# Kernel tuning notes

Measured on AMD Instinct MI355X. Metric: run time of the kernel, lower is better.

The kernel has to match this reference:

```python
import jax, jax.numpy as jnp
from jax import lax
import numpy as np

WINDOW_SIZE = 11
SIGMA = 1.5  # create_windows hardcodes 1.5, ignoring self.sigma
C1 = 0.01 ** 2
C2 = 0.03 ** 2


def _gaussian(ws, sigma):
    x = np.arange(ws, dtype=np.float32)
    g = np.exp(-((x - ws // 2) ** 2) / (2.0 * sigma ** 2))
    return (g / g.sum()).astype(np.float32)


def _blur(x, window):
    # Separable depthwise Gaussian blur with 'same' symmetric padding.
    # x: [N, 1, H, W]; window: [ws]
    ws = window.shape[0]
    p = ws // 2
    dn = ('NCHW', 'OIHW', 'NCHW')
    kh = window.reshape(1, 1, ws, 1)
    kw = window.reshape(1, 1, 1, ws)
    x = lax.conv_general_dilated(x, kh, (1, 1), [(p, p), (0, 0)], dimension_numbers=dn)
    x = lax.conv_general_dilated(x, kw, (1, 1), [(0, 0), (p, p)], dimension_numbers=dn)
    return x


def setup_inputs() -> dict:
    key = jax.random.key(0)
    k1, k2 = jax.random.split(key)
    shape = (16, 1, 1024, 1024)
    img1 = jax.random.uniform(k1, shape, dtype=jnp.float32)
    img2 = jax.random.uniform(k2, shape, dtype=jnp.float32)
    window = jnp.asarray(_gaussian(WINDOW_SIZE, SIGMA))
    return {"img1": img1, "img2": img2, "window": window}


def reference(img1, img2, window):
    mu1 = _blur(img1, window)
    mu2 = _blur(img2, window)
    mu1_sq = mu1 * mu1
    mu2_sq = mu2 * mu2
    mu1_mu2 = mu1 * mu2
    sigma1_sq = _blur(img1 * img1, window) - mu1_sq
    sigma2_sq = _blur(img2 * img2, window) - mu2_sq
    sigma12 = _blur(img1 * img2, window) - mu1_mu2
    ssim_map = ((2.0 * mu1_mu2 + C1) * (2.0 * sigma12 + C2)) / (
        (mu1_sq + mu2_sq + C1) * (sigma1_sq + sigma2_sq + C2))
    return jnp.mean(ssim_map)  # size_average=True
```

## Files before the change

### kernel.cpp

```cpp
#include <hip/hip_runtime.h>


typedef float f4 __attribute__((ext_vector_type(4)));

#define W      1024
#define H      1024
#define NIMG   16
#define HALO   5
#define TW     64
#define TOW    54
#define RPS    8
#define NSTG   4
#define TH     (RPS*NSTG)
#define NTX    19
#define NTY    (H/TH)
#define WPB    8
#define BX     (WPB*64)
#define NWAVE  (NTX*NTY*NIMG)
#define NBLK   (NWAVE/WPB)

template<bool INT>
__device__ __forceinline__ void pf_row(const float* __restrict__ p1,
                                       const float* __restrict__ p2,
                                       int j, int c, bool cOK,
                                       float& a, float& b)
{
    if (INT) {
        a = p1[(size_t)j * W + c];
        b = p2[(size_t)j * W + c];
    } else {
        const bool ok = cOK && ((unsigned)j < H);
        a = ok ? p1[(size_t)j * W + c] : 0.0f;
        b = ok ? p2[(size_t)j * W + c] : 0.0f;
    }
}

__device__ __forceinline__ f4 pack_ch(float a, float b)
{
    f4 v;
    v.x = a; v.y = b;
    v.z = fmaf(a, a, b * b);
    v.w = a * b;
    return v;
}

template<bool INT>
__device__ float wave_tile(const float* __restrict__ p1,
                           const float* __restrict__ p2,
                           const float* __restrict__ w,
                           int cb, int r0, int lane, int obase,
                           f4 (*lds)[TW])
{
    const int  c   = cb + lane;
    const bool cOK = INT || ((unsigned)c < W);

    f4 ring[11];
#pragma unroll
    for (int k = 0; k < 10; ++k) {
        float a, b;
        pf_row<INT>(p1, p2, r0 - HALO + k, c, cOK, a, b);
        ring[k + 1] = pack_ch(a, b);
    }

    const int q   = lane >> 3;
    const int run = lane & 7;
    const int S0  = (run < 7) ? 7 * run : 47;

    float pa[RPS], pb[RPS];
#pragma unroll
    for (int rr = 0; rr < RPS; ++rr)
        pf_row<INT>(p1, p2, r0 + HALO + rr, c, cOK, pa[rr], pb[rr]);

    float tsum = 0.0f;

    for (int st = 0; st < NSTG; ++st) {
#pragma unroll
        for (int rr = 0; rr < RPS; ++rr) {
#pragma unroll
            for (int k = 0; k < 10; ++k) ring[k] = ring[k + 1];
            ring[10] = pack_ch(pa[rr], pb[rr]);

            f4 acc = w[5] * ring[5];
#pragma unroll
            for (int k = 0; k < 5; ++k)
                acc += w[k] * (ring[k] + ring[10 - k]);

            lds[rr][lane] = acc;
        }

        if (st + 1 < NSTG) {
#pragma unroll
            for (int rr = 0; rr < RPS; ++rr)
                pf_row<INT>(p1, p2, r0 + (st + 1) * RPS + HALO + rr, c, cOK,
                            pa[rr], pb[rr]);
        }

        {
            f4 o[7] = {};
#pragma unroll
            for (int i = 0; i < 17; ++i) {
                const f4 u = lds[q][S0 + i];
#pragma unroll
                for (int oo = 0; oo < 7; ++oo) {
                    const int k = i - oo;
                    if (k >= 0 && k < 11)
                        o[oo] += w[k] * u;
                }
            }

            const float C1f = 0.0001f, C2f = 0.0009f;
#pragma unroll
            for (int oo = 0; oo < 7; ++oo) {
                const int rel = S0 + oo;
                const bool valid = ((run < 7) || (oo >= 2)) &&
                                   (INT || (obase + rel) < W);
                if (valid) {
                    const float m1 = o[oo].x, m2 = o[oo].y;
                    const float qq = o[oo].z, pp = o[oo].w;
                    const float mu12 = m1 * m2, m1s = m1 * m1, m2s = m2 * m2;
                    const float s12 = pp - mu12;
                    const float ssq = qq - m1s - m2s;
                    const float num = (2.f * mu12 + C1f) * (2.f * s12 + C2f);
                    const float den = (m1s + m2s + C1f) * (ssq + C2f);
                    tsum += num * __builtin_amdgcn_rcpf(den);
                }
            }
        }
    }
    return tsum;
}

__global__ __launch_bounds__(BX) void ssim_main(const float* __restrict__ img1,
                                                const float* __restrict__ img2,
                                                const float* __restrict__ win,
                                                float* __restrict__ partials)
{
    __shared__ f4 lds[WPB][RPS][TW];

    const int t    = threadIdx.x;
    const int wid  = t >> 6;
    const int lane = t & 63;
    const int gw   = blockIdx.x * WPB + wid;

    const int img = gw / (NTX * NTY);
    const int rem = gw - img * (NTX * NTY);
    const int gy  = rem / NTX;
    const int tx  = rem - gy * NTX;

    const int cb    = tx * TOW - HALO;
    const int obase = tx * TOW;
    const int r0    = gy * TH;

    const float* __restrict__ p1 = img1 + (size_t)img * (size_t)(W * H);
    const float* __restrict__ p2 = img2 + (size_t)img * (size_t)(W * H);

    float w[11];
#pragma unroll
    for (int k = 0; k < 11; ++k)
        w[k] = __int_as_float(__builtin_amdgcn_readfirstlane(__float_as_int(win[k])));

    const bool interior = (cb >= 0) && (cb + TW <= W) &&
                          (r0 >= HALO) && (r0 + TH - 1 + HALO < H);

    float tsum = interior
               ? wave_tile<true >(p1, p2, w, cb, r0, lane, obase, lds[wid])
               : wave_tile<false>(p1, p2, w, cb, r0, lane, obase, lds[wid]);

#pragma unroll
    for (int off = 32; off > 0; off >>= 1)
        tsum += __shfl_down(tsum, off, 64);

    if (lane == 0)
        partials[gw] = tsum;
}

__global__ __launch_bounds__(256) void ssim_finalize(const float* __restrict__ partials,
                                                     float* __restrict__ out)
{
    double s = 0.0;
    for (int i = threadIdx.x; i < NWAVE; i += 256) s += (double)partials[i];
#pragma unroll
    for (int off = 32; off > 0; off >>= 1)
        s += __shfl_down(s, off, 64);

    __shared__ double ws[4];
    if ((threadIdx.x & 63) == 0) ws[threadIdx.x >> 6] = s;
    __syncthreads();
    if (threadIdx.x == 0) {
        const double tt = ws[0] + ws[1] + ws[2] + ws[3];
        out[0] = (float)(tt / (double)((size_t)NIMG * W * H));
    }
}

extern "C" void kernel_launch(void* const* d_in, const int* in_sizes, int n_in,
                              void* d_out, int out_size, void* d_ws, size_t ws_size,
                              hipStream_t stream)
{
    const float* img1 = (const float*)d_in[0];
    const float* img2 = (const float*)d_in[1];
    const float* win  = (const float*)d_in[2];
    float* partials   = (float*)d_ws;
    float* out        = (float*)d_out;

    ssim_main<<<NBLK, BX, 0, stream>>>(img1, img2, win, partials);
    ssim_finalize<<<1, 256, 0, stream>>>(partials, out);
}
```

Before: 66.29 us.

## Use packed FP32 math for separable blur and enlarge per-wave tile height

Rewrites the vertical and horizontal Gaussian accumulations to use v_pk_add/mul/fma_f32 inline asm on float2 pairs, with the weights broadcast into both halves, so each packed instruction does two FMAs. It also doubles the stages per wave (taller tiles, which cuts redundant vertical halo reads) and halves waves per block. The inline asm hides the operations from the compiler's scheduler and makes it keep the weights in VGPR pairs, which may raise register pressure. Fewer, taller tiles also mean less parallelism.

```diff
diff --git a/kernel.cpp b/kernel.cpp
--- a/kernel.cpp
+++ b/kernel.cpp
@@ -1,6 +1,7 @@
 #include <hip/hip_runtime.h>
 
 
+typedef float f2 __attribute__((ext_vector_type(2)));
 typedef float f4 __attribute__((ext_vector_type(4)));
 
 #define W      1024
@@ -10,14 +11,31 @@
 #define TW     64
 #define TOW    54
 #define RPS    8
-#define NSTG   4
+#define NSTG   8
 #define TH     (RPS*NSTG)
 #define NTX    19
 #define NTY    (H/TH)
-#define WPB    8
+#define WPB    4
 #define BX     (WPB*64)
 #define NWAVE  (NTX*NTY*NIMG)
 #define NBLK   (NWAVE/WPB)
+
+__device__ __forceinline__ f2 pk_add(f2 a, f2 b)
+{
+    f2 d;
+    asm("v_pk_add_f32 %0, %1, %2" : "=v"(d) : "v"(a), "v"(b));
+    return d;
+}
+__device__ __forceinline__ f2 pk_mul(f2 a, f2 b)
+{
+    f2 d;
+    asm("v_pk_mul_f32 %0, %1, %2" : "=v"(d) : "v"(a), "v"(b));
+    return d;
+}
+__device__ __forceinline__ void pk_fma(f2& acc, f2 a, f2 b)
+{
+    asm("v_pk_fma_f32 %0, %1, %2, %0" : "+v"(acc) : "v"(a), "v"(b));
+}
 
 template<bool INT>
 __device__ __forceinline__ void pf_row(const float* __restrict__ p1,
@@ -35,31 +53,23 @@
     }
 }
 
-__device__ __forceinline__ f4 pack_ch(float a, float b)
-{
-    f4 v;
-    v.x = a; v.y = b;
-    v.z = fmaf(a, a, b * b);
-    v.w = a * b;
-    return v;
-}
-
 template<bool INT>
 __device__ float wave_tile(const float* __restrict__ p1,
                            const float* __restrict__ p2,
-                           const float* __restrict__ w,
+                           const f2* __restrict__ w2,
                            int cb, int r0, int lane, int obase,
                            f4 (*lds)[TW])
 {
     const int  c   = cb + lane;
     const bool cOK = INT || ((unsigned)c < W);
 
-    f4 ring[11];
+    f2 rAB[11], rQP[11];
 #pragma unroll
     for (int k = 0; k < 10; ++k) {
         float a, b;
         pf_row<INT>(p1, p2, r0 - HALO + k, c, cOK, a, b);
-        ring[k + 1] = pack_ch(a, b);
+        rAB[k + 1].x = a;              rAB[k + 1].y = b;
+        rQP[k + 1].x = fmaf(a, a, b * b); rQP[k + 1].y = a * b;
     }
 
     const int q   = lane >> 3;
@@ -77,15 +87,24 @@
 #pragma unroll
         for (int rr = 0; rr < RPS; ++rr) {
 #pragma unroll
-            for (int k = 0; k < 10; ++k) ring[k] = ring[k + 1];
-            ring[10] = pack_ch(pa[rr], pb[rr]);
-
-            f4 acc = w[5] * ring[5];
-#pragma unroll
-            for (int k = 0; k < 5; ++k)
-                acc += w[k] * (ring[k] + ring[10 - k]);
-
-            lds[rr][lane] = acc;
+            for (int k = 0; k < 10; ++k) { rAB[k] = rAB[k + 1]; rQP[k] = rQP[k + 1]; }
+            {
+                const float a = pa[rr], b = pb[rr];
+                rAB[10].x = a;               rAB[10].y = b;
+                rQP[10].x = fmaf(a, a, b * b); rQP[10].y = a * b;
+            }
+
+            f2 vAB = pk_mul(w2[5], rAB[5]);
+            f2 vQP = pk_mul(w2[5], rQP[5]);
+#pragma unroll
+            for (int k = 0; k < 5; ++k) {
+                pk_fma(vAB, w2[k], pk_add(rAB[k], rAB[10 - k]));
+                pk_fma(vQP, w2[k], pk_add(rQP[k], rQP[10 - k]));
+            }
+
+            f4 v;
+            v.x = vAB.x; v.y = vAB.y; v.z = vQP.x; v.w = vQP.y;
+            lds[rr][lane] = v;
         }
 
         if (st + 1 < NSTG) {
@@ -96,15 +115,19 @@
         }
 
         {
-            f4 o[7] = {};
+            f2 oAB[7] = {}, oQP[7] = {};
 #pragma unroll
             for (int i = 0; i < 17; ++i) {
                 const f4 u = lds[q][S0 + i];
+                const f2 uAB = __builtin_shufflevector(u, u, 0, 1);
+                const f2 uQP = __builtin_shufflevector(u, u, 2, 3);
 #pragma unroll
                 for (int oo = 0; oo < 7; ++oo) {
                     const int k = i - oo;
-                    if (k >= 0 && k < 11)
-                        o[oo] += w[k] * u;
+                    if (k >= 0 && k < 11) {
+                        pk_fma(oAB[oo], w2[k], uAB);
+                        pk_fma(oQP[oo], w2[k], uQP);
+                    }
                 }
             }
 
@@ -115,8 +138,8 @@
                 const bool valid = ((run < 7) || (oo >= 2)) &&
                                    (INT || (obase + rel) < W);
                 if (valid) {
-                    const float m1 = o[oo].x, m2 = o[oo].y;
-                    const float qq = o[oo].z, pp = o[oo].w;
+                    const float m1 = oAB[oo].x, m2 = oAB[oo].y;
+                    const float qq = oQP[oo].x, pp = oQP[oo].y;
                     const float mu12 = m1 * m2, m1s = m1 * m1, m2s = m2 * m2;
                     const float s12 = pp - mu12;
                     const float ssq = qq - m1s - m2s;
@@ -154,17 +177,20 @@
     const float* __restrict__ p1 = img1 + (size_t)img * (size_t)(W * H);
     const float* __restrict__ p2 = img2 + (size_t)img * (size_t)(W * H);
 
-    float w[11];
-#pragma unroll
-    for (int k = 0; k < 11; ++k)
-        w[k] = __int_as_float(__builtin_amdgcn_readfirstlane(__float_as_int(win[k])));
+    f2 w2[11];
+#pragma unroll
+    for (int k = 0; k < 11; ++k) {
+        const float wk =
+            __int_as_float(__builtin_amdgcn_readfirstlane(__float_as_int(win[k])));
+        w2[k].x = wk; w2[k].y = wk;
+    }
 
     const bool interior = (cb >= 0) && (cb + TW <= W) &&
                           (r0 >= HALO) && (r0 + TH - 1 + HALO < H);
 
     float tsum = interior
-               ? wave_tile<true >(p1, p2, w, cb, r0, lane, obase, lds[wid])
-               : wave_tile<false>(p1, p2, w, cb, r0, lane, obase, lds[wid]);
+               ? wave_tile<true >(p1, p2, w2, cb, r0, lane, obase, lds[wid])
+               : wave_tile<false>(p1, p2, w2, cb, r0, lane, obase, lds[wid]);
 
 #pragma unroll
     for (int off = 32; off > 0; off >>= 1)
```

After: 64.48 us. 1.03x faster.

## Process two row-tiles per wave to add independent work and ILP

Applied to the files above, without the earlier changes.

Each wave now computes two vertically separated tiles (top and bottom halves of the image) at once, interleaving their loads, vertical passes and horizontal passes. Blocks shrink from 8 waves to 2, and the number of waves is halved. The goal is more memory-level parallelism and instruction-level overlap within a wave. In exchange, register pressure doubles (two rings and two prefetch sets), which may lower occupancy, and fewer waves are launched.

```diff
diff --git a/kernel.cpp b/kernel.cpp
--- a/kernel.cpp
+++ b/kernel.cpp
@@ -13,11 +13,11 @@
 #define NSTG   4
 #define TH     (RPS*NSTG)
 #define NTX    19
-#define NTY    (H/TH)
-#define WPB    8
+#define NTYH   16
+#define NSLOT  (NTX*NTYH*NIMG)
+#define WPB    2
 #define BX     (WPB*64)
-#define NWAVE  (NTX*NTY*NIMG)
-#define NBLK   (NWAVE/WPB)
+#define NBLK   (NSLOT/WPB)
 
 template<bool INT>
 __device__ __forceinline__ void pf_row(const float* __restrict__ p1,
@@ -44,88 +44,112 @@
     return v;
 }
 
+__device__ __forceinline__ void vstage(const float* __restrict__ w,
+                                       const float (&pa)[RPS], const float (&pb)[RPS],
+                                       f4 (&ring)[11], f4 (*slab)[TW], int lane)
+{
+#pragma unroll
+    for (int rr = 0; rr < RPS; ++rr) {
+#pragma unroll
+        for (int k = 0; k < 10; ++k) ring[k] = ring[k + 1];
+        ring[10] = pack_ch(pa[rr], pb[rr]);
+
+        f4 acc = w[5] * ring[5];
+#pragma unroll
+        for (int k = 0; k < 5; ++k)
+            acc += w[k] * (ring[k] + ring[10 - k]);
+
+        slab[rr][lane] = acc;
+    }
+}
+
 template<bool INT>
-__device__ float wave_tile(const float* __restrict__ p1,
+__device__ __forceinline__ float hstage(const float* __restrict__ w,
+                                        const f4 (*slab)[TW],
+                                        int q, int run, int S0, int obase)
+{
+    f4 o[7] = {};
+#pragma unroll
+    for (int i = 0; i < 17; ++i) {
+        const f4 u = slab[q][S0 + i];
+#pragma unroll
+        for (int oo = 0; oo < 7; ++oo) {
+            const int k = i - oo;
+            if (k >= 0 && k < 11)
+                o[oo] += w[k] * u;
+        }
+    }
+
+    float s = 0.0f;
+    const float C1f = 0.0001f, C2f = 0.0009f;
+#pragma unroll
+    for (int oo = 0; oo < 7; ++oo) {
+        const int rel = S0 + oo;
+        const bool valid = ((run < 7) || (oo >= 2)) &&
+                           (INT || (obase + rel) < W);
+        if (valid) {
+            const float m1 = o[oo].x, m2 = o[oo].y;
+            const float qq = o[oo].z, pp = o[oo].w;
+            const float mu12 = m1 * m2, m1s = m1 * m1, m2s = m2 * m2;
+            const float s12 = pp - mu12;
+            const float ssq = qq - m1s - m2s;
+            const float num = (2.f * mu12 + C1f) * (2.f * s12 + C2f);
+            const float den = (m1s + m2s + C1f) * (ssq + C2f);
+            s += num * __builtin_amdgcn_rcpf(den);
+        }
+    }
+    return s;
+}
+
+template<bool INT>
+__device__ float wave_pair(const float* __restrict__ p1,
                            const float* __restrict__ p2,
                            const float* __restrict__ w,
-                           int cb, int r0, int lane, int obase,
-                           f4 (*lds)[TW])
+                           int cb, int rA0, int rB0, int lane, int obase,
+                           f4 (*slabA)[TW], f4 (*slabB)[TW])
 {
     const int  c   = cb + lane;
     const bool cOK = INT || ((unsigned)c < W);
 
-    f4 ring[11];
+    f4 ringA[11], ringB[11];
 #pragma unroll
     for (int k = 0; k < 10; ++k) {
         float a, b;
-        pf_row<INT>(p1, p2, r0 - HALO + k, c, cOK, a, b);
-        ring[k + 1] = pack_ch(a, b);
+        pf_row<INT>(p1, p2, rA0 - HALO + k, c, cOK, a, b);
+        ringA[k + 1] = pack_ch(a, b);
+        pf_row<INT>(p1, p2, rB0 - HALO + k, c, cOK, a, b);
+        ringB[k + 1] = pack_ch(a, b);
     }
 
     const int q   = lane >> 3;
     const int run = lane & 7;
     const int S0  = (run < 7) ? 7 * run : 47;
 
-    float pa[RPS], pb[RPS];
-#pragma unroll
-    for (int rr = 0; rr < RPS; ++rr)
-        pf_row<INT>(p1, p2, r0 + HALO + rr, c, cOK, pa[rr], pb[rr]);
+    float paA[RPS], pbA[RPS], paB[RPS], pbB[RPS];
+#pragma unroll
+    for (int rr = 0; rr < RPS; ++rr) {
+        pf_row<INT>(p1, p2, rA0 + HALO + rr, c, cOK, paA[rr], pbA[rr]);
+        pf_row<INT>(p1, p2, rB0 + HALO + rr, c, cOK, paB[rr], pbB[rr]);
+    }
 
     float tsum = 0.0f;
 
     for (int st = 0; st < NSTG; ++st) {
-#pragma unroll
-        for (int rr = 0; rr < RPS; ++rr) {
-#pragma unroll
-            for (int k = 0; k < 10; ++k) ring[k] = ring[k + 1];
-            ring[10] = pack_ch(pa[rr], pb[rr]);
-
-            f4 acc = w[5] * ring[5];
-#pragma unroll
-            for (int k = 0; k < 5; ++k)
-                acc += w[k] * (ring[k] + ring[10 - k]);
-
-            lds[rr][lane] = acc;
-        }
+        vstage(w, paA, pbA, ringA, slabA, lane);
+        vstage(w, paB, pbB, ringB, slabB, lane);
 
         if (st + 1 < NSTG) {
 #pragma unroll
-            for (int rr = 0; rr < RPS; ++rr)
-                pf_row<INT>(p1, p2, r0 + (st + 1) * RPS + HALO + rr, c, cOK,
-                            pa[rr], pb[rr]);
-        }
-
-        {
-            f4 o[7] = {};
-#pragma unroll
-            for (int i = 0; i < 17; ++i) {
-                const f4 u = lds[q][S0 + i];
-#pragma unroll
-                for (int oo = 0; oo < 7; ++oo) {
-                    const int k = i - oo;
-                    if (k >= 0 && k < 11)
-                        o[oo] += w[k] * u;
-                }
-            }
-
-            const float C1f = 0.0001f, C2f = 0.0009f;
-#pragma unroll
-            for (int oo = 0; oo < 7; ++oo) {
-                const int rel = S0 + oo;
-                const bool valid = ((run < 7) || (oo >= 2)) &&
-                                   (INT || (obase + rel) < W);
-                if (valid) {
-                    const float m1 = o[oo].x, m2 = o[oo].y;
-                    const float qq = o[oo].z, pp = o[oo].w;
-                    const float mu12 = m1 * m2, m1s = m1 * m1, m2s = m2 * m2;
-                    const float s12 = pp - mu12;
-                    const float ssq = qq - m1s - m2s;
-                    const float num = (2.f * mu12 + C1f) * (2.f * s12 + C2f);
-                    const float den = (m1s + m2s + C1f) * (ssq + C2f);
-                    tsum += num * __builtin_amdgcn_rcpf(den);
-                }
+            for (int rr = 0; rr < RPS; ++rr) {
+                pf_row<INT>(p1, p2, rA0 + (st + 1) * RPS + HALO + rr, c, cOK,
+                            paA[rr], pbA[rr]);
+                pf_row<INT>(p1, p2, rB0 + (st + 1) * RPS + HALO + rr, c, cOK,
+                            paB[rr], pbB[rr]);
             }
         }
+
+        tsum += hstage<INT>(w, slabA, q, run, S0, obase);
+        tsum += hstage<INT>(w, slabB, q, run, S0, obase);
     }
     return tsum;
 }
@@ -135,21 +159,22 @@
                                                 const float* __restrict__ win,
                                                 float* __restrict__ partials)
 {
-    __shared__ f4 lds[WPB][RPS][TW];
+    __shared__ f4 lds[WPB][2][RPS][TW];
 
     const int t    = threadIdx.x;
     const int wid  = t >> 6;
     const int lane = t & 63;
     const int gw   = blockIdx.x * WPB + wid;
 
-    const int img = gw / (NTX * NTY);
-    const int rem = gw - img * (NTX * NTY);
-    const int gy  = rem / NTX;
-    const int tx  = rem - gy * NTX;
+    const int img = gw / (NTX * NTYH);
+    const int rem = gw - img * (NTX * NTYH);
+    const int gyA = rem / NTX;
+    const int tx  = rem - gyA * NTX;
 
     const int cb    = tx * TOW - HALO;
     const int obase = tx * TOW;
-    const int r0    = gy * TH;
+    const int rA0   = gyA * TH;
+    const int rB0   = rA0 + NTYH * TH;
 
     const float* __restrict__ p1 = img1 + (size_t)img * (size_t)(W * H);
     const float* __restrict__ p2 = img2 + (size_t)img * (size_t)(W * H);
@@ -160,11 +185,13 @@
         w[k] = __int_as_float(__builtin_amdgcn_readfirstlane(__float_as_int(win[k])));
 
     const bool interior = (cb >= 0) && (cb + TW <= W) &&
-                          (r0 >= HALO) && (r0 + TH - 1 + HALO < H);
+                          (rA0 >= HALO) && (rB0 + TH - 1 + HALO < H);
 
     float tsum = interior
-               ? wave_tile<true >(p1, p2, w, cb, r0, lane, obase, lds[wid])
-               : wave_tile<false>(p1, p2, w, cb, r0, lane, obase, lds[wid]);
+               ? wave_pair<true >(p1, p2, w, cb, rA0, rB0, lane, obase,
+                                  lds[wid][0], lds[wid][1])
+               : wave_pair<false>(p1, p2, w, cb, rA0, rB0, lane, obase,
+                                  lds[wid][0], lds[wid][1]);
 
 #pragma unroll
     for (int off = 32; off > 0; off >>= 1)
@@ -178,7 +205,7 @@
                                                      float* __restrict__ out)
 {
     double s = 0.0;
-    for (int i = threadIdx.x; i < NWAVE; i += 256) s += (double)partials[i];
+    for (int i = threadIdx.x; i < NSLOT; i += 256) s += (double)partials[i];
 #pragma unroll
     for (int off = 32; off > 0; off >>= 1)
         s += __shfl_down(s, off, 64);
```

Result: slower. 71.39 us (+7.7%).

## Double-buffer LDS stages and interleave vertical/horizontal passes with prefetch

Applied to the files above, without the earlier changes.

Adds a double-buffered LDS stage so each stage's vertical blur writes into the next buffer while the horizontal blur of the previous stage is interleaved row by row, with global prefetches issued per row. Also doubles the stages per wave (taller tiles, less halo recompute) and reduces waves per block from eight to two. The aim is to hide LDS and global latency within a wave and to cut redundant halo rows. The cost is more registers and LDS per wave, and fewer total waves, which lowers parallelism.

```diff
diff --git a/kernel.cpp b/kernel.cpp
--- a/kernel.cpp
+++ b/kernel.cpp
@@ -10,11 +10,11 @@
 #define TW     64
 #define TOW    54
 #define RPS    8
-#define NSTG   4
+#define NSTG   8
 #define TH     (RPS*NSTG)
 #define NTX    19
 #define NTY    (H/TH)
-#define WPB    8
+#define WPB    2
 #define BX     (WPB*64)
 #define NWAVE  (NTX*NTY*NIMG)
 #define NBLK   (NWAVE/WPB)
@@ -45,11 +45,36 @@
 }
 
 template<bool INT>
+__device__ __forceinline__ float ssim_epi(const f4 (&o)[7], int run, int S0,
+                                          int obase)
+{
+    float s = 0.0f;
+    const float C1f = 0.0001f, C2f = 0.0009f;
+#pragma unroll
+    for (int oo = 0; oo < 7; ++oo) {
+        const int rel = S0 + oo;
+        const bool valid = ((run < 7) || (oo >= 2)) &&
+                           (INT || (obase + rel) < W);
+        if (valid) {
+            const float m1 = o[oo].x, m2 = o[oo].y;
+            const float qq = o[oo].z, pp = o[oo].w;
+            const float mu12 = m1 * m2, m1s = m1 * m1, m2s = m2 * m2;
+            const float s12 = pp - mu12;
+            const float ssq = qq - m1s - m2s;
+            const float num = (2.f * mu12 + C1f) * (2.f * s12 + C2f);
+            const float den = (m1s + m2s + C1f) * (ssq + C2f);
+            s += num * __builtin_amdgcn_rcpf(den);
+        }
+    }
+    return s;
+}
+
+template<bool INT>
 __device__ float wave_tile(const float* __restrict__ p1,
                            const float* __restrict__ p2,
                            const float* __restrict__ w,
                            int cb, int r0, int lane, int obase,
-                           f4 (*lds)[TW])
+                           f4 (*lds)[RPS][TW])
 {
     const int  c   = cb + lane;
     const bool cOK = INT || ((unsigned)c < W);
@@ -70,63 +95,89 @@
 #pragma unroll
     for (int rr = 0; rr < RPS; ++rr)
         pf_row<INT>(p1, p2, r0 + HALO + rr, c, cOK, pa[rr], pb[rr]);
+#pragma unroll
+    for (int rr = 0; rr < RPS; ++rr) {
+#pragma unroll
+        for (int k = 0; k < 10; ++k) ring[k] = ring[k + 1];
+        ring[10] = pack_ch(pa[rr], pb[rr]);
+        f4 acc = w[5] * ring[5];
+#pragma unroll
+        for (int k = 0; k < 5; ++k)
+            acc += w[k] * (ring[k] + ring[10 - k]);
+        lds[0][rr][lane] = acc;
+    }
+#pragma unroll
+    for (int rr = 0; rr < RPS; ++rr)
+        pf_row<INT>(p1, p2, r0 + RPS + HALO + rr, c, cOK, pa[rr], pb[rr]);
 
     float tsum = 0.0f;
 
-    for (int st = 0; st < NSTG; ++st) {
+    for (int st = 0; st < NSTG - 1; ++st) {
+        const f4 (*ob)[TW] = (const f4 (*)[TW])lds[st & 1];
+        f4 (*nb)[TW] = lds[(st + 1) & 1];
+        const int  pfrow  = r0 + (st + 2) * RPS + HALO;
+        const bool lastpf = (st + 2 >= NSTG);
+
+        f4 o[7] = {};
+
 #pragma unroll
         for (int rr = 0; rr < RPS; ++rr) {
+            const int i0 = 2 * rr;
+            const int i1 = (rr == 7) ? 17 : (2 * rr + 2);
+
+            f4 u[3];
+#pragma unroll
+            for (int i = 0; i < 3; ++i)
+                if (i0 + i < i1)
+                    u[i] = ob[q][S0 + i0 + i];
+
 #pragma unroll
             for (int k = 0; k < 10; ++k) ring[k] = ring[k + 1];
             ring[10] = pack_ch(pa[rr], pb[rr]);
-
             f4 acc = w[5] * ring[5];
 #pragma unroll
             for (int k = 0; k < 5; ++k)
                 acc += w[k] * (ring[k] + ring[10 - k]);
-
-            lds[rr][lane] = acc;
-        }
-
-        if (st + 1 < NSTG) {
-#pragma unroll
-            for (int rr = 0; rr < RPS; ++rr)
-                pf_row<INT>(p1, p2, r0 + (st + 1) * RPS + HALO + rr, c, cOK,
-                            pa[rr], pb[rr]);
-        }
-
-        {
-            f4 o[7] = {};
-#pragma unroll
-            for (int i = 0; i < 17; ++i) {
-                const f4 u = lds[q][S0 + i];
-#pragma unroll
-                for (int oo = 0; oo < 7; ++oo) {
-                    const int k = i - oo;
-                    if (k >= 0 && k < 11)
-                        o[oo] += w[k] * u;
-                }
+            nb[rr][lane] = acc;
+
+            {
+                const int j = lastpf ? r0 : (pfrow + rr);
+                pf_row<INT>(p1, p2, j, c, cOK, pa[rr], pb[rr]);
             }
 
-            const float C1f = 0.0001f, C2f = 0.0009f;
-#pragma unroll
-            for (int oo = 0; oo < 7; ++oo) {
-                const int rel = S0 + oo;
-                const bool valid = ((run < 7) || (oo >= 2)) &&
-                                   (INT || (obase + rel) < W);
-                if (valid) {
-                    const float m1 = o[oo].x, m2 = o[oo].y;
-                    const float qq = o[oo].z, pp = o[oo].w;
-                    const float mu12 = m1 * m2, m1s = m1 * m1, m2s = m2 * m2;
-                    const float s12 = pp - mu12;
-                    const float ssq = qq - m1s - m2s;
-                    const float num = (2.f * mu12 + C1f) * (2.f * s12 + C2f);
-                    const float den = (m1s + m2s + C1f) * (ssq + C2f);
-                    tsum += num * __builtin_amdgcn_rcpf(den);
+#pragma unroll
+            for (int i = 0; i < 3; ++i) {
+                const int ii = i0 + i;
+                if (ii < i1) {
+#pragma unroll
+                    for (int oo = 0; oo < 7; ++oo) {
+                        const int k = ii - oo;
+                        if (k >= 0 && k < 11)
+                            o[oo] += w[k] * u[i];
+                    }
                 }
             }
         }
-    }
+
+        tsum += ssim_epi<INT>(o, run, S0, obase);
+    }
+
+    {
+        const f4 (*ob)[TW] = (const f4 (*)[TW])lds[(NSTG - 1) & 1];
+        f4 o[7] = {};
+#pragma unroll
+        for (int i = 0; i < 17; ++i) {
+            const f4 u = ob[q][S0 + i];
+#pragma unroll
+            for (int oo = 0; oo < 7; ++oo) {
+                const int k = i - oo;
+                if (k >= 0 && k < 11)
+                    o[oo] += w[k] * u;
+            }
+        }
+        tsum += ssim_epi<INT>(o, run, S0, obase);
+    }
+
     return tsum;
 }
 
@@ -135,7 +186,7 @@
                                                 const float* __restrict__ win,
                                                 float* __restrict__ partials)
 {
-    __shared__ f4 lds[WPB][RPS][TW];
+    __shared__ f4 lds[WPB][2][RPS][TW];
 
     const int t    = threadIdx.x;
     const int wid  = t >> 6;
```

After: 74.16 us. +11.9%, slower.
